# Kernel tuning notes

Hardware: AMD Instinct MI355X
Metric: run time of the kernel (lower is better)

Reference implementation:

```python
import jax, jax.numpy as jnp
import numpy as np

HIDDEN = 512
INPUT = 256
P_VALUE = 0.2
EPS = 0.001


def setup_inputs() -> dict:
    key = jax.random.key(0)
    k1, k2, k3, k4 = jax.random.split(key, 4)
    stdv = 1.0 / np.sqrt(HIDDEN)
    inputs = jax.random.normal(k1, (64, 1024, INPUT), dtype=jnp.float32)
    weight_ih = jax.random.uniform(k2, (3 * HIDDEN, INPUT), jnp.float32, -stdv, stdv)
    weight_hh = jax.random.uniform(k3, (3 * HIDDEN, HIDDEN), jnp.float32, -stdv, stdv)
    bias = jax.random.uniform(k4, (3 * HIDDEN,), jnp.float32, -stdv, stdv)
    return {"inputs": inputs, "weight_ih": weight_ih, "weight_hh": weight_hh, "bias": bias}


def reference(inputs, weight_ih, weight_hh, bias):
    # inputs: [B, T, I] (batch_first). hidden=None -> h=c=0, k=-1.
    B, T, _ = inputs.shape
    H = weight_hh.shape[1]
    h0 = jnp.zeros((B, H), inputs.dtype)
    c0 = jnp.zeros((B, H), inputs.dtype)
    k0 = -jnp.ones((B, H), inputs.dtype)
    p_t = jnp.asarray(P_VALUE, inputs.dtype)  # learn_p=False: constant p

    def step(state, xt):
        h, c, k = state
        x, t = xt  # x: [B, I], t: scalar timestep
        gates = x @ weight_ih.T + h @ weight_hh.T + bias  # [B, 3H]
        r, o, g = jnp.split(gates, 3, axis=1)
        r = jax.nn.sigmoid(r)
        o = jax.nn.sigmoid(o)
        g = jnp.tanh(g)
        k_new = r * (t - EPS) + (1.0 - r) * k
        f = jnp.power((t - k_new + EPS) / (t - k_new + 1.0), p_t)
        c_new = f * c + (1.0 - f) * g
        h_new = o * jnp.tanh(c_new)
        return (h_new, c_new, k_new), h_new

    ts = jnp.arange(T, dtype=inputs.dtype)
    xs = jnp.transpose(inputs, (1, 0, 2))  # [T, B, I]
    (h_f, c_f, k_f), hs = jax.lax.scan(step, (h0, c0, k0), (xs, ts))
    out = jnp.transpose(hs, (1, 0, 2))  # [B, T, H]
    return out, h_f, c_f, k_f
```

## Files before the change

kernel.cpp:

```cpp
#include <hip/hip_runtime.h>
#include <stdint.h>
#include <stddef.h>


#define Hh   512
#define Tt   1024
#define Bb   64
#define II   256
#define EPSc 0.001f
#define PV   0.2f

typedef unsigned long long u64;

__global__ __launch_bounds__(1024) void plr_init(u64* hbuf2) {
  int idx = blockIdx.x * blockDim.x + threadIdx.x;
  hbuf2[idx] = 0ull;
  hbuf2[idx + 32768] = 0ull;
}

__global__ __launch_bounds__(512, 2)
void plr_main(
    const float* __restrict__ x,
    const float* __restrict__ Wih,
    const float* __restrict__ Whh,
    const float* __restrict__ bias,
    float* __restrict__ out,
    u64* hbuf2)
{
  __shared__ float h_tile[8 * Hh];
  __shared__ float x_tile[2 * 8 * II];
  __shared__ float part[2 * 3264];

  const int tid = threadIdx.x;
  const int w   = tid >> 6;
  const int l   = tid & 63;
  const int jj  = l & 15;
  const int kc  = (w << 2) | ((l >> 4) & 3);
  const int bid = blockIdx.x;
  const int g   = bid & 7;
  const int s   = bid >> 3;
  const int j0  = s * 16;
  const int b0  = g * 8;
  const int jw  = w << 6;
  const int bls = l >> 3;
  const int xk  = (w << 5) + (l & 7) * 4;

  float whh[3][16];
  float wih[3][8];
#pragma unroll
  for (int gi = 0; gi < 3; ++gi) {
    const int row = gi * Hh + j0 + jj;
    const float4* ph = (const float4*)(Whh + (size_t)row * Hh + kc * 16);
#pragma unroll
    for (int i = 0; i < 4; ++i) {
      float4 v = ph[i];
      whh[gi][4*i+0] = v.x; whh[gi][4*i+1] = v.y;
      whh[gi][4*i+2] = v.z; whh[gi][4*i+3] = v.w;
    }
    const float4* pi = (const float4*)(Wih + (size_t)row * II + kc * 8);
#pragma unroll
    for (int i = 0; i < 2; ++i) {
      float4 v = pi[i];
      wih[gi][4*i+0] = v.x; wih[gi][4*i+1] = v.y;
      wih[gi][4*i+2] = v.z; wih[gi][4*i+3] = v.w;
    }
  }

  float c_st = 0.0f, k_st = -1.0f;
  float bia0 = 0.f, bia1 = 0.f, bia2 = 0.f;
  if (tid < 128) {
    const int jr = tid & 15;
    bia0 = bias[0 * Hh + j0 + jr];
    bia1 = bias[1 * Hh + j0 + jr];
    bia2 = bias[2 * Hh + j0 + jr];
  }

  *(float4*)(x_tile + bls * II + xk) =
      *(const float4*)(x + ((size_t)(b0 + bls) * Tt + 0) * II + xk);

  bool broken = false;

  for (int t = 0; t < Tt; ++t) {
    const u64* hb = hbuf2 + (size_t)(t & 1) * Bb * Hh + (size_t)b0 * Hh;
    u64 got[8];
#pragma unroll
    for (int i = 0; i < 8; ++i)
      got[i] = __hip_atomic_load(hb + (size_t)i * Hh + jw + l,
                                 __ATOMIC_RELAXED, __HIP_MEMORY_SCOPE_AGENT);

    const float* xt = x_tile + (t & 1) * 8 * II;
    float xacc[3][8];
#pragma unroll
    for (int bl = 0; bl < 8; ++bl) {
      const float4* x4 = (const float4*)(xt + bl * II) + kc * 2;
      float a0 = 0.f, a1 = 0.f, a2 = 0.f;
#pragma unroll
      for (int i = 0; i < 2; ++i) {
        float4 xv = x4[i];
        a0 = fmaf(wih[0][4*i+0], xv.x, a0); a0 = fmaf(wih[0][4*i+1], xv.y, a0);
        a0 = fmaf(wih[0][4*i+2], xv.z, a0); a0 = fmaf(wih[0][4*i+3], xv.w, a0);
        a1 = fmaf(wih[1][4*i+0], xv.x, a1); a1 = fmaf(wih[1][4*i+1], xv.y, a1);
        a1 = fmaf(wih[1][4*i+2], xv.z, a1); a1 = fmaf(wih[1][4*i+3], xv.w, a1);
        a2 = fmaf(wih[2][4*i+0], xv.x, a2); a2 = fmaf(wih[2][4*i+1], xv.y, a2);
        a2 = fmaf(wih[2][4*i+2], xv.z, a2); a2 = fmaf(wih[2][4*i+3], xv.w, a2);
      }
      xacc[0][bl] = a0; xacc[1][bl] = a1; xacc[2][bl] = a2;
    }

    {
      const unsigned want = (unsigned)t;
      int it = 0;
      for (;;) {
        bool ok = true;
#pragma unroll
        for (int i = 0; i < 8; ++i) ok &= ((unsigned)(got[i] >> 32) == want);
        if (__all((int)ok)) break;
        if (++it > (1 << 20)) { broken = true; break; }
        __builtin_amdgcn_s_sleep(1);
#pragma unroll
        for (int i = 0; i < 8; ++i)
          if ((unsigned)(got[i] >> 32) != want)
            got[i] = __hip_atomic_load(hb + (size_t)i * Hh + jw + l,
                                       __ATOMIC_RELAXED,
                                       __HIP_MEMORY_SCOPE_AGENT);
      }
    }

#pragma unroll
    for (int i = 0; i < 8; ++i)
      h_tile[i * Hh + jw + l] = __uint_as_float((unsigned)got[i]);

    float* pb = part + (t & 1) * 3264;
#pragma unroll
    for (int pass = 0; pass < 2; ++pass) {
      float acc[3][4];
#pragma unroll
      for (int b4 = 0; b4 < 4; ++b4) {
        const int bl = pass * 4 + b4;
        const float4* h4 = (const float4*)(h_tile + bl * Hh) + kc * 4;
        float a0 = xacc[0][bl], a1 = xacc[1][bl], a2 = xacc[2][bl];
#pragma unroll
        for (int i = 0; i < 4; ++i) {
          float4 hv = h4[i];
          a0 = fmaf(whh[0][4*i+0], hv.x, a0); a0 = fmaf(whh[0][4*i+1], hv.y, a0);
          a0 = fmaf(whh[0][4*i+2], hv.z, a0); a0 = fmaf(whh[0][4*i+3], hv.w, a0);
          a1 = fmaf(whh[1][4*i+0], hv.x, a1); a1 = fmaf(whh[1][4*i+1], hv.y, a1);
          a1 = fmaf(whh[1][4*i+2], hv.z, a1); a1 = fmaf(whh[1][4*i+3], hv.w, a1);
          a2 = fmaf(whh[2][4*i+0], hv.x, a2); a2 = fmaf(whh[2][4*i+1], hv.y, a2);
          a2 = fmaf(whh[2][4*i+2], hv.z, a2); a2 = fmaf(whh[2][4*i+3], hv.w, a2);
        }
        acc[0][b4] = a0; acc[1][b4] = a1; acc[2][b4] = a2;
      }
#pragma unroll
      for (int gi = 0; gi < 3; ++gi)
#pragma unroll
        for (int b4 = 0; b4 < 4; ++b4) {
          float v = acc[gi][b4];
          v += __shfl_xor(v, 16, 64);
          v += __shfl_xor(v, 32, 64);
          if (l < 16)
            pb[((gi * 8 + pass * 4 + b4) * 8 + w) * 17 + jj] = v;
        }
    }

    if (t + 1 < Tt)
      *(float4*)(x_tile + ((t + 1) & 1) * 8 * II + bls * II + xk) =
          *(const float4*)(x + ((size_t)(b0 + bls) * Tt + (t + 1)) * II + xk);

    __syncthreads();

    if (tid < 128) {
      const int jr = tid & 15, br = tid >> 4;
      float s0 = bia0, s1 = bia1, s2 = bia2;
#pragma unroll
      for (int ww = 0; ww < 8; ++ww) {
        s0 += pb[((0 * 8 + br) * 8 + ww) * 17 + jr];
        s1 += pb[((1 * 8 + br) * 8 + ww) * 17 + jr];
        s2 += pb[((2 * 8 + br) * 8 + ww) * 17 + jr];
      }
      const float tf = (float)t;
      const float r  = 1.0f / (1.0f + __expf(-s0));
      const float o  = 1.0f / (1.0f + __expf(-s1));
      const float gg = 1.0f - 2.0f / (1.0f + __expf(2.0f * s2));
      const float kn = r * (tf - EPSc) + (1.0f - r) * k_st;
      const float d  = tf - kn;
      const float f  = __expf(PV * __logf((d + EPSc) / (d + 1.0f)));
      const float cn = f * c_st + (1.0f - f) * gg;
      const float hn = o * (1.0f - 2.0f / (1.0f + __expf(2.0f * cn)));
      c_st = cn; k_st = kn;

      if (t + 1 < Tt) {
        u64* hp = hbuf2 + (size_t)((t + 1) & 1) * Bb * Hh +
                  (size_t)(b0 + br) * Hh + j0 + jr;
        u64 atom = ((u64)(unsigned)(t + 1) << 32) |
                   (u64)__float_as_uint(hn);
        __hip_atomic_store(hp, atom, __ATOMIC_RELAXED,
                           __HIP_MEMORY_SCOPE_AGENT);
      }

      const int b = b0 + br, j = j0 + jr;
      out[((size_t)b * Tt + t) * Hh + j] = hn;
      if (t == Tt - 1) {
        const size_t base = (size_t)Bb * Tt * Hh;
        out[base + 0 * Bb * Hh + (size_t)b * Hh + j] = hn;
        out[base + 1 * Bb * Hh + (size_t)b * Hh + j] = cn;
        out[base + 2 * Bb * Hh + (size_t)b * Hh + j] = kn;
      }
    }
  }
  (void)broken;
}

extern "C" void kernel_launch(void* const* d_in, const int* in_sizes, int n_in,
                              void* d_out, int out_size, void* d_ws, size_t ws_size,
                              hipStream_t stream) {
  const float* x    = (const float*)d_in[0];
  const float* Wih  = (const float*)d_in[1];
  const float* Whh  = (const float*)d_in[2];
  const float* bias = (const float*)d_in[3];
  float* out = (float*)d_out;

  u64* hbuf2 = (u64*)d_ws;

  plr_init<<<32, 1024, 0, stream>>>(hbuf2);
  plr_main<<<256, 512, 0, stream>>>(x, Wih, Whh, bias, out, hbuf2);
}
```

Before: 5.620 ms.

## Split gate epilogue into a dedicated wavefront and prefetch next x into registers

Adds a ninth wavefront per block that handles only the partial-sum reduction, the gate nonlinearities, the h/c/k state update, publishing h and writing the outputs, with each of its threads covering two batch rows. The eight compute wavefronts now skip that epilogue and go straight on to the next step's input projection and spin-wait while it runs. The next timestep's x slice is loaded into registers at the top of the iteration so its global latency overlaps the spin-wait and matvec. The cost is a larger block of 576 threads with the same launch-bounds occupancy target, which may squeeze the register budget, and a longer per-thread epilogue on the critical recurrence path.

```diff
diff --git a/kernel.cpp b/kernel.cpp
--- a/kernel.cpp
+++ b/kernel.cpp
@@ -18,7 +18,7 @@
   hbuf2[idx + 32768] = 0ull;
 }
 
-__global__ __launch_bounds__(512, 2)
+__global__ __launch_bounds__(576, 2)
 void plr_main(
     const float* __restrict__ x,
     const float* __restrict__ Wih,
@@ -32,183 +32,209 @@
   __shared__ float part[2 * 3264];
 
   const int tid = threadIdx.x;
-  const int w   = tid >> 6;
-  const int l   = tid & 63;
-  const int jj  = l & 15;
-  const int kc  = (w << 2) | ((l >> 4) & 3);
   const int bid = blockIdx.x;
   const int g   = bid & 7;
   const int s   = bid >> 3;
   const int j0  = s * 16;
   const int b0  = g * 8;
-  const int jw  = w << 6;
-  const int bls = l >> 3;
-  const int xk  = (w << 5) + (l & 7) * 4;
-
-  float whh[3][16];
-  float wih[3][8];
-#pragma unroll
-  for (int gi = 0; gi < 3; ++gi) {
-    const int row = gi * Hh + j0 + jj;
-    const float4* ph = (const float4*)(Whh + (size_t)row * Hh + kc * 16);
-#pragma unroll
-    for (int i = 0; i < 4; ++i) {
-      float4 v = ph[i];
-      whh[gi][4*i+0] = v.x; whh[gi][4*i+1] = v.y;
-      whh[gi][4*i+2] = v.z; whh[gi][4*i+3] = v.w;
+
+  if (tid < 512) {
+    const int w   = tid >> 6;
+    const int l   = tid & 63;
+    const int jj  = l & 15;
+    const int kc  = (w << 2) | ((l >> 4) & 3);
+    const int jw  = w << 6;
+    const int bls = l >> 3;
+    const int xk  = (w << 5) + (l & 7) * 4;
+
+    float whh[3][16];
+    float wih[3][8];
+#pragma unroll
+    for (int gi = 0; gi < 3; ++gi) {
+      const int row = gi * Hh + j0 + jj;
+      const float4* ph = (const float4*)(Whh + (size_t)row * Hh + kc * 16);
+#pragma unroll
+      for (int i = 0; i < 4; ++i) {
+        float4 v = ph[i];
+        whh[gi][4*i+0] = v.x; whh[gi][4*i+1] = v.y;
+        whh[gi][4*i+2] = v.z; whh[gi][4*i+3] = v.w;
+      }
+      const float4* pi = (const float4*)(Wih + (size_t)row * II + kc * 8);
+#pragma unroll
+      for (int i = 0; i < 2; ++i) {
+        float4 v = pi[i];
+        wih[gi][4*i+0] = v.x; wih[gi][4*i+1] = v.y;
+        wih[gi][4*i+2] = v.z; wih[gi][4*i+3] = v.w;
+      }
     }
-    const float4* pi = (const float4*)(Wih + (size_t)row * II + kc * 8);
-#pragma unroll
-    for (int i = 0; i < 2; ++i) {
-      float4 v = pi[i];
-      wih[gi][4*i+0] = v.x; wih[gi][4*i+1] = v.y;
-      wih[gi][4*i+2] = v.z; wih[gi][4*i+3] = v.w;
+
+    *(float4*)(x_tile + bls * II + xk) =
+        *(const float4*)(x + ((size_t)(b0 + bls) * Tt + 0) * II + xk);
+
+    bool broken = false;
+
+    for (int t = 0; t < Tt; ++t) {
+      float4 xreg = make_float4(0.f, 0.f, 0.f, 0.f);
+      if (t + 1 < Tt)
+        xreg = *(const float4*)(x + ((size_t)(b0 + bls) * Tt + (t + 1)) * II + xk);
+
+      const u64* hb = hbuf2 + (size_t)(t & 1) * Bb * Hh + (size_t)b0 * Hh;
+      u64 got[8];
+#pragma unroll
+      for (int i = 0; i < 8; ++i)
+        got[i] = __hip_atomic_load(hb + (size_t)i * Hh + jw + l,
+                                   __ATOMIC_RELAXED, __HIP_MEMORY_SCOPE_AGENT);
+
+      const float* xt = x_tile + (t & 1) * 8 * II;
+      float xacc[3][8];
+#pragma unroll
+      for (int bl = 0; bl < 8; ++bl) {
+        const float4* x4 = (const float4*)(xt + bl * II) + kc * 2;
+        float a0 = 0.f, a1 = 0.f, a2 = 0.f;
+#pragma unroll
+        for (int i = 0; i < 2; ++i) {
+          float4 xv = x4[i];
+          a0 = fmaf(wih[0][4*i+0], xv.x, a0); a0 = fmaf(wih[0][4*i+1], xv.y, a0);
+          a0 = fmaf(wih[0][4*i+2], xv.z, a0); a0 = fmaf(wih[0][4*i+3], xv.w, a0);
+          a1 = fmaf(wih[1][4*i+0], xv.x, a1); a1 = fmaf(wih[1][4*i+1], xv.y, a1);
+          a1 = fmaf(wih[1][4*i+2], xv.z, a1); a1 = fmaf(wih[1][4*i+3], xv.w, a1);
+          a2 = fmaf(wih[2][4*i+0], xv.x, a2); a2 = fmaf(wih[2][4*i+1], xv.y, a2);
+          a2 = fmaf(wih[2][4*i+2], xv.z, a2); a2 = fmaf(wih[2][4*i+3], xv.w, a2);
+        }
+        xacc[0][bl] = a0; xacc[1][bl] = a1; xacc[2][bl] = a2;
+      }
+
+      {
+        const unsigned want = (unsigned)t;
+        int it = 0;
+        for (;;) {
+          bool ok = true;
+#pragma unroll
+          for (int i = 0; i < 8; ++i) ok &= ((unsigned)(got[i] >> 32) == want);
+          if (__all((int)ok)) break;
+          if (++it > (1 << 20)) { broken = true; break; }
+          __builtin_amdgcn_s_sleep(1);
+#pragma unroll
+          for (int i = 0; i < 8; ++i)
+            if ((unsigned)(got[i] >> 32) != want)
+              got[i] = __hip_atomic_load(hb + (size_t)i * Hh + jw + l,
+                                         __ATOMIC_RELAXED,
+                                         __HIP_MEMORY_SCOPE_AGENT);
+        }
+      }
+
+#pragma unroll
+      for (int i = 0; i < 8; ++i)
+        h_tile[i * Hh + jw + l] = __uint_as_float((unsigned)got[i]);
+
+      float* pb = part + (t & 1) * 3264;
+#pragma unroll
+      for (int pass = 0; pass < 2; ++pass) {
+        float acc[3][4];
+#pragma unroll
+        for (int b4 = 0; b4 < 4; ++b4) {
+          const int bl = pass * 4 + b4;
+          const float4* h4 = (const float4*)(h_tile + bl * Hh) + kc * 4;
+          float a0 = xacc[0][bl], a1 = xacc[1][bl], a2 = xacc[2][bl];
+#pragma unroll
+          for (int i = 0; i < 4; ++i) {
+            float4 hv = h4[i];
+            a0 = fmaf(whh[0][4*i+0], hv.x, a0); a0 = fmaf(whh[0][4*i+1], hv.y, a0);
+            a0 = fmaf(whh[0][4*i+2], hv.z, a0); a0 = fmaf(whh[0][4*i+3], hv.w, a0);
+            a1 = fmaf(whh[1][4*i+0], hv.x, a1); a1 = fmaf(whh[1][4*i+1], hv.y, a1);
+            a1 = fmaf(whh[1][4*i+2], hv.z, a1); a1 = fmaf(whh[1][4*i+3], hv.w, a1);
+            a2 = fmaf(whh[2][4*i+0], hv.x, a2); a2 = fmaf(whh[2][4*i+1], hv.y, a2);
+            a2 = fmaf(whh[2][4*i+2], hv.z, a2); a2 = fmaf(whh[2][4*i+3], hv.w, a2);
+          }
+          acc[0][b4] = a0; acc[1][b4] = a1; acc[2][b4] = a2;
+        }
+#pragma unroll
+        for (int gi = 0; gi < 3; ++gi)
+#pragma unroll
+          for (int b4 = 0; b4 < 4; ++b4) {
+            float v = acc[gi][b4];
+            v += __shfl_xor(v, 16, 64);
+            v += __shfl_xor(v, 32, 64);
+            if (l < 16)
+              pb[((gi * 8 + pass * 4 + b4) * 8 + w) * 17 + jj] = v;
+          }
+      }
+
+      if (t + 1 < Tt)
+        *(float4*)(x_tile + ((t + 1) & 1) * 8 * II + bls * II + xk) = xreg;
+
+      __syncthreads();
+    }
+    (void)broken;
+
+  } else {
+    const int u   = tid - 512;
+    const int jr  = u & 15;
+    const int br0 = u >> 4;
+    const float bia0 = bias[0 * Hh + j0 + jr];
+    const float bia1 = bias[1 * Hh + j0 + jr];
+    const float bia2 = bias[2 * Hh + j0 + jr];
+    float c0 = 0.f, k0 = -1.f, c1 = 0.f, k1 = -1.f;
+
+    for (int t = 0; t < Tt; ++t) {
+      __syncthreads();
+
+      const float* pb = part + (t & 1) * 3264;
+      float s00 = bia0, s01 = bia1, s02 = bia2;
+      float s10 = bia0, s11 = bia1, s12 = bia2;
+#pragma unroll
+      for (int ww = 0; ww < 8; ++ww) {
+        s00 += pb[((0 * 8 + br0) * 8 + ww) * 17 + jr];
+        s01 += pb[((1 * 8 + br0) * 8 + ww) * 17 + jr];
+        s02 += pb[((2 * 8 + br0) * 8 + ww) * 17 + jr];
+        s10 += pb[((0 * 8 + br0 + 4) * 8 + ww) * 17 + jr];
+        s11 += pb[((1 * 8 + br0 + 4) * 8 + ww) * 17 + jr];
+        s12 += pb[((2 * 8 + br0 + 4) * 8 + ww) * 17 + jr];
+      }
+
+      const float tf = (float)t;
+      const float r0  = 1.0f / (1.0f + __expf(-s00));
+      const float r1  = 1.0f / (1.0f + __expf(-s10));
+      const float o0  = 1.0f / (1.0f + __expf(-s01));
+      const float o1  = 1.0f / (1.0f + __expf(-s11));
+      const float gg0 = 1.0f - 2.0f / (1.0f + __expf(2.0f * s02));
+      const float gg1 = 1.0f - 2.0f / (1.0f + __expf(2.0f * s12));
+      const float kn0 = r0 * (tf - EPSc) + (1.0f - r0) * k0;
+      const float kn1 = r1 * (tf - EPSc) + (1.0f - r1) * k1;
+      const float d0  = tf - kn0;
+      const float d1  = tf - kn1;
+      const float f0  = __expf(PV * __logf((d0 + EPSc) / (d0 + 1.0f)));
+      const float f1  = __expf(PV * __logf((d1 + EPSc) / (d1 + 1.0f)));
+      const float cn0 = f0 * c0 + (1.0f - f0) * gg0;
+      const float cn1 = f1 * c1 + (1.0f - f1) * gg1;
+      const float hn0 = o0 * (1.0f - 2.0f / (1.0f + __expf(2.0f * cn0)));
+      const float hn1 = o1 * (1.0f - 2.0f / (1.0f + __expf(2.0f * cn1)));
+      c0 = cn0; k0 = kn0; c1 = cn1; k1 = kn1;
+
+      if (t + 1 < Tt) {
+        u64* hp = hbuf2 + (size_t)((t + 1) & 1) * Bb * Hh;
+        u64 a0 = ((u64)(unsigned)(t + 1) << 32) | (u64)__float_as_uint(hn0);
+        u64 a1 = ((u64)(unsigned)(t + 1) << 32) | (u64)__float_as_uint(hn1);
+        __hip_atomic_store(hp + (size_t)(b0 + br0) * Hh + j0 + jr, a0,
+                           __ATOMIC_RELAXED, __HIP_MEMORY_SCOPE_AGENT);
+        __hip_atomic_store(hp + (size_t)(b0 + br0 + 4) * Hh + j0 + jr, a1,
+                           __ATOMIC_RELAXED, __HIP_MEMORY_SCOPE_AGENT);
+      }
+
+      const int bA = b0 + br0, bB = b0 + br0 + 4, j = j0 + jr;
+      out[((size_t)bA * Tt + t) * Hh + j] = hn0;
+      out[((size_t)bB * Tt + t) * Hh + j] = hn1;
+      if (t == Tt - 1) {
+        const size_t base = (size_t)Bb * Tt * Hh;
+        out[base + 0 * Bb * Hh + (size_t)bA * Hh + j] = hn0;
+        out[base + 1 * Bb * Hh + (size_t)bA * Hh + j] = cn0;
+        out[base + 2 * Bb * Hh + (size_t)bA * Hh + j] = kn0;
+        out[base + 0 * Bb * Hh + (size_t)bB * Hh + j] = hn1;
+        out[base + 1 * Bb * Hh + (size_t)bB * Hh + j] = cn1;
+        out[base + 2 * Bb * Hh + (size_t)bB * Hh + j] = kn1;
+      }
     }
   }
-
-  float c_st = 0.0f, k_st = -1.0f;
-  float bia0 = 0.f, bia1 = 0.f, bia2 = 0.f;
-  if (tid < 128) {
-    const int jr = tid & 15;
-    bia0 = bias[0 * Hh + j0 + jr];
-    bia1 = bias[1 * Hh + j0 + jr];
-    bia2 = bias[2 * Hh + j0 + jr];
-  }
-
-  *(float4*)(x_tile + bls * II + xk) =
-      *(const float4*)(x + ((size_t)(b0 + bls) * Tt + 0) * II + xk);
-
-  bool broken = false;
-
-  for (int t = 0; t < Tt; ++t) {
-    const u64* hb = hbuf2 + (size_t)(t & 1) * Bb * Hh + (size_t)b0 * Hh;
-    u64 got[8];
-#pragma unroll
-    for (int i = 0; i < 8; ++i)
-      got[i] = __hip_atomic_load(hb + (size_t)i * Hh + jw + l,
-                                 __ATOMIC_RELAXED, __HIP_MEMORY_SCOPE_AGENT);
-
-    const float* xt = x_tile + (t & 1) * 8 * II;
-    float xacc[3][8];
-#pragma unroll
-    for (int bl = 0; bl < 8; ++bl) {
-      const float4* x4 = (const float4*)(xt + bl * II) + kc * 2;
-      float a0 = 0.f, a1 = 0.f, a2 = 0.f;
-#pragma unroll
-      for (int i = 0; i < 2; ++i) {
-        float4 xv = x4[i];
-        a0 = fmaf(wih[0][4*i+0], xv.x, a0); a0 = fmaf(wih[0][4*i+1], xv.y, a0);
-        a0 = fmaf(wih[0][4*i+2], xv.z, a0); a0 = fmaf(wih[0][4*i+3], xv.w, a0);
-        a1 = fmaf(wih[1][4*i+0], xv.x, a1); a1 = fmaf(wih[1][4*i+1], xv.y, a1);
-        a1 = fmaf(wih[1][4*i+2], xv.z, a1); a1 = fmaf(wih[1][4*i+3], xv.w, a1);
-        a2 = fmaf(wih[2][4*i+0], xv.x, a2); a2 = fmaf(wih[2][4*i+1], xv.y, a2);
-        a2 = fmaf(wih[2][4*i+2], xv.z, a2); a2 = fmaf(wih[2][4*i+3], xv.w, a2);
-      }
-      xacc[0][bl] = a0; xacc[1][bl] = a1; xacc[2][bl] = a2;
-    }
-
-    {
-      const unsigned want = (unsigned)t;
-      int it = 0;
-      for (;;) {
-        bool ok = true;
-#pragma unroll
-        for (int i = 0; i < 8; ++i) ok &= ((unsigned)(got[i] >> 32) == want);
-        if (__all((int)ok)) break;
-        if (++it > (1 << 20)) { broken = true; break; }
-        __builtin_amdgcn_s_sleep(1);
-#pragma unroll
-        for (int i = 0; i < 8; ++i)
-          if ((unsigned)(got[i] >> 32) != want)
-            got[i] = __hip_atomic_load(hb + (size_t)i * Hh + jw + l,
-                                       __ATOMIC_RELAXED,
-                                       __HIP_MEMORY_SCOPE_AGENT);
-      }
-    }
-
-#pragma unroll
-    for (int i = 0; i < 8; ++i)
-      h_tile[i * Hh + jw + l] = __uint_as_float((unsigned)got[i]);
-
-    float* pb = part + (t & 1) * 3264;
-#pragma unroll
-    for (int pass = 0; pass < 2; ++pass) {
-      float acc[3][4];
-#pragma unroll
-      for (int b4 = 0; b4 < 4; ++b4) {
-        const int bl = pass * 4 + b4;
-        const float4* h4 = (const float4*)(h_tile + bl * Hh) + kc * 4;
-        float a0 = xacc[0][bl], a1 = xacc[1][bl], a2 = xacc[2][bl];
-#pragma unroll
-        for (int i = 0; i < 4; ++i) {
-          float4 hv = h4[i];
-          a0 = fmaf(whh[0][4*i+0], hv.x, a0); a0 = fmaf(whh[0][4*i+1], hv.y, a0);
-          a0 = fmaf(whh[0][4*i+2], hv.z, a0); a0 = fmaf(whh[0][4*i+3], hv.w, a0);
-          a1 = fmaf(whh[1][4*i+0], hv.x, a1); a1 = fmaf(whh[1][4*i+1], hv.y, a1);
-          a1 = fmaf(whh[1][4*i+2], hv.z, a1); a1 = fmaf(whh[1][4*i+3], hv.w, a1);
-          a2 = fmaf(whh[2][4*i+0], hv.x, a2); a2 = fmaf(whh[2][4*i+1], hv.y, a2);
-          a2 = fmaf(whh[2][4*i+2], hv.z, a2); a2 = fmaf(whh[2][4*i+3], hv.w, a2);
-        }
-        acc[0][b4] = a0; acc[1][b4] = a1; acc[2][b4] = a2;
-      }
-#pragma unroll
-      for (int gi = 0; gi < 3; ++gi)
-#pragma unroll
-        for (int b4 = 0; b4 < 4; ++b4) {
-          float v = acc[gi][b4];
-          v += __shfl_xor(v, 16, 64);
-          v += __shfl_xor(v, 32, 64);
-          if (l < 16)
-            pb[((gi * 8 + pass * 4 + b4) * 8 + w) * 17 + jj] = v;
-        }
-    }
-
-    if (t + 1 < Tt)
-      *(float4*)(x_tile + ((t + 1) & 1) * 8 * II + bls * II + xk) =
-          *(const float4*)(x + ((size_t)(b0 + bls) * Tt + (t + 1)) * II + xk);
-
-    __syncthreads();
-
-    if (tid < 128) {
-      const int jr = tid & 15, br = tid >> 4;
-      float s0 = bia0, s1 = bia1, s2 = bia2;
-#pragma unroll
-      for (int ww = 0; ww < 8; ++ww) {
-        s0 += pb[((0 * 8 + br) * 8 + ww) * 17 + jr];
-        s1 += pb[((1 * 8 + br) * 8 + ww) * 17 + jr];
-        s2 += pb[((2 * 8 + br) * 8 + ww) * 17 + jr];
-      }
-      const float tf = (float)t;
-      const float r  = 1.0f / (1.0f + __expf(-s0));
-      const float o  = 1.0f / (1.0f + __expf(-s1));
-      const float gg = 1.0f - 2.0f / (1.0f + __expf(2.0f * s2));
-      const float kn = r * (tf - EPSc) + (1.0f - r) * k_st;
-      const float d  = tf - kn;
-      const float f  = __expf(PV * __logf((d + EPSc) / (d + 1.0f)));
-      const float cn = f * c_st + (1.0f - f) * gg;
-      const float hn = o * (1.0f - 2.0f / (1.0f + __expf(2.0f * cn)));
-      c_st = cn; k_st = kn;
-
-      if (t + 1 < Tt) {
-        u64* hp = hbuf2 + (size_t)((t + 1) & 1) * Bb * Hh +
-                  (size_t)(b0 + br) * Hh + j0 + jr;
-        u64 atom = ((u64)(unsigned)(t + 1) << 32) |
-                   (u64)__float_as_uint(hn);
-        __hip_atomic_store(hp, atom, __ATOMIC_RELAXED,
-                           __HIP_MEMORY_SCOPE_AGENT);
-      }
-
-      const int b = b0 + br, j = j0 + jr;
-      out[((size_t)b * Tt + t) * Hh + j] = hn;
-      if (t == Tt - 1) {
-        const size_t base = (size_t)Bb * Tt * Hh;
-        out[base + 0 * Bb * Hh + (size_t)b * Hh + j] = hn;
-        out[base + 1 * Bb * Hh + (size_t)b * Hh + j] = cn;
-        out[base + 2 * Bb * Hh + (size_t)b * Hh + j] = kn;
-      }
-    }
-  }
-  (void)broken;
 }
 
 extern "C" void kernel_launch(void* const* d_in, const int* in_sizes, int n_in,
@@ -223,5 +249,5 @@
   u64* hbuf2 = (u64*)d_ws;
 
   plr_init<<<32, 1024, 0, stream>>>(hbuf2);
-  plr_main<<<256, 512, 0, stream>>>(x, Wih, Whh, bias, out, hbuf2);
+  plr_main<<<256, 576, 0, stream>>>(x, Wih, Whh, bias, out, hbuf2);
 }
```

Result: slower. 15.43 ms (+174.6%).
